# Performance work log

Hardware: AMD Instinct MI355X
Metric: run time of the kernel (lower is better)

The kernel has to match this reference:

```python
import jax, jax.numpy as jnp
import numpy as np

C = 1280  # layers_dim[1]


def setup_inputs() -> dict:
    key = jax.random.key(0)
    ks = jax.random.split(key, 8)
    E, N, H, W = 8192, 1024, 4, 4
    pose = jax.random.normal(ks[0], (E, 9), dtype=jnp.float32)
    image = jax.random.normal(ks[1], (N, C, H, W), dtype=jnp.float32)
    # edge_encoder params: Linear(9,1280) -> ReLU -> Linear(1280,2560) -> Sigmoid
    W1 = jax.random.normal(ks[2], (9, C), dtype=jnp.float32) * (1.0 / np.sqrt(9))
    b1 = jnp.zeros((C,), dtype=jnp.float32)
    W2 = jax.random.normal(ks[3], (C, 2 * C), dtype=jnp.float32) * (1.0 / np.sqrt(C))
    b2 = jnp.zeros((2 * C,), dtype=jnp.float32)
    src = jax.random.randint(ks[4], (E,), 0, N)
    dst = jax.random.randint(ks[5], (E,), 0, N)
    return {"pose": pose, "image": image, "W1": W1, "b1": b1,
            "W2": W2, "b2": b2, "src": src, "dst": dst}


def reference(pose, image, W1, b1, W2, b2, src, dst):
    # edge encoder: MLP -> sigmoid -> interleaved (gamma, beta) per channel
    h = jax.nn.relu(pose @ W1 + b1)                        # [E, C]
    e = jax.nn.sigmoid(h @ W2 + b2).reshape(-1, C, 2)      # [E, C, 2]
    gamma = e[:, :, 0][:, :, None, None]                   # [E, C, 1, 1]
    beta = e[:, :, 1][:, :, None, None]                    # [E, C, 1, 1]
    # per-edge message: affine transform of source node feature map
    m = gamma * image[src] + beta                          # [E, C, H, W]
    N = image.shape[0]
    s = jax.ops.segment_sum(m, dst, num_segments=N)        # [N, C, H, W]
    cnt = jax.ops.segment_sum(jnp.ones((m.shape[0],), m.dtype), dst,
                              num_segments=N)              # [N]
    cnt4 = cnt[:, None, None, None]
    # mean over mailbox; nodes with no incoming edges stay zero (DGL default)
    return jnp.where(cnt4 > 0, s / jnp.maximum(cnt4, 1.0), 0.0)
```

## Files before the change

kernel.cpp:

```cpp
#include <hip/hip_runtime.h>

#define C_DIM 1280
#define K_DIM 1280
#define N_DIM 2560
#define HWSZ 16
#define CHW (C_DIM*HWSZ)

#define BM 128
#define BN 128
#define BK 64
#define NT (K_DIM / BK)

#define EPB 32
#define NBC 2048

typedef __bf16 bf16;
typedef __attribute__((ext_vector_type(8))) __bf16 bf16x8;
typedef __attribute__((ext_vector_type(4))) __bf16 bf16x4;
typedef __attribute__((ext_vector_type(8))) unsigned short u16x8;
typedef __attribute__((ext_vector_type(4))) float f32x4;

__device__ __forceinline__ void gload_lds16(const void* g, void* l) {
  __builtin_amdgcn_global_load_lds(
      (const __attribute__((address_space(1))) void*)g,
      (__attribute__((address_space(3))) void*)l, 16, 0, 0);
}

__global__ __launch_bounds__(256) void prep(
    const float* __restrict__ pose, const float* __restrict__ W1,
    const float* __restrict__ b1, bf16* __restrict__ h,
    const float* __restrict__ W2, bf16* __restrict__ W2t,
    const float* __restrict__ img32, bf16* __restrict__ imgb,
    const int* __restrict__ dst, const int* __restrict__ src,
    int* __restrict__ offsets, int2* __restrict__ pairs, int E, int N)
{
  const int b = blockIdx.x;
  const int t = threadIdx.x;
  const int NBP = (E / EPB) * 5;
  const int NBT = (N_DIM / 32) * (K_DIM / 32);

  if (b == 0) {
    __shared__ int cnt[1024];
    __shared__ int cur[1024];
    __shared__ int wsum[4];
    #pragma unroll
    for (int i = 0; i < 4; ++i) cnt[t + 256 * i] = 0;
    __syncthreads();
    const int4* dst4 = (const int4*)dst;
    const int4* src4 = (const int4*)src;
    const int E4 = E >> 2;
    for (int e4 = t; e4 < E4; e4 += 256) {
      const int4 d = dst4[e4];
      atomicAdd(&cnt[d.x], 1); atomicAdd(&cnt[d.y], 1);
      atomicAdd(&cnt[d.z], 1); atomicAdd(&cnt[d.w], 1);
    }
    __syncthreads();
    const int s0 = cnt[4*t], s1 = cnt[4*t+1], s2 = cnt[4*t+2], s3 = cnt[4*t+3];
    const int tot = s0 + s1 + s2 + s3;
    const int lane = t & 63, w = t >> 6;
    int x = tot;
    #pragma unroll
    for (int off = 1; off < 64; off <<= 1) {
      int y = __shfl_up(x, off);
      if (lane >= off) x += y;
    }
    if (lane == 63) wsum[w] = x;
    __syncthreads();
    int woff = 0;
    for (int i = 0; i < w; ++i) woff += wsum[i];
    const int excl = x + woff - tot;
    const int o0 = excl, o1 = o0 + s0, o2 = o1 + s1, o3 = o2 + s2;
    offsets[4*t] = o0; offsets[4*t+1] = o1; offsets[4*t+2] = o2; offsets[4*t+3] = o3;
    cur[4*t] = o0; cur[4*t+1] = o1; cur[4*t+2] = o2; cur[4*t+3] = o3;
    if (t == 0) offsets[N] = E;
    __syncthreads();
    for (int e4 = t; e4 < E4; e4 += 256) {
      const int4 d = dst4[e4];
      const int4 s = src4[e4];
      const int e = e4 * 4;
      int p;
      p = atomicAdd(&cur[d.x], 1); pairs[p] = make_int2(e,     s.x);
      p = atomicAdd(&cur[d.y], 1); pairs[p] = make_int2(e + 1, s.y);
      p = atomicAdd(&cur[d.z], 1); pairs[p] = make_int2(e + 2, s.z);
      p = atomicAdd(&cur[d.w], 1); pairs[p] = make_int2(e + 3, s.w);
    }
    return;
  }

  const int pb = b - 1;
  if (pb < NBP) {
    const int eg = pb / 5;
    const int cc = pb % 5;
    const int c  = cc * 256 + t;
    const int e0 = eg * EPB;
    float w[9];
    #pragma unroll
    for (int k = 0; k < 9; ++k) w[k] = W1[k * C_DIM + c];
    const float bias = b1[c];
    #pragma unroll 4
    for (int i = 0; i < EPB; ++i) {
      const float* p = pose + (size_t)(e0 + i) * 9;
      float s = bias;
      #pragma unroll
      for (int k = 0; k < 9; ++k) s += p[k] * w[k];
      s = s > 0.f ? s : 0.f;
      h[(size_t)(e0 + i) * C_DIM + c] = (bf16)s;
    }
    return;
  }

  if (pb < NBP + NBT) {
    const int tb = pb - NBP;
    __shared__ float tile[32][33];
    const int n0 = (tb % (N_DIM / 32)) * 32;
    const int k0 = (tb / (N_DIM / 32)) * 32;
    const int r  = t >> 3;
    const int c4 = (t & 7) * 4;
    const f32x4 v = *(const f32x4*)(W2 + (size_t)(k0 + r) * N_DIM + n0 + c4);
    tile[r][c4] = v[0]; tile[r][c4+1] = v[1]; tile[r][c4+2] = v[2]; tile[r][c4+3] = v[3];
    __syncthreads();
    bf16x4 o;
    o[0] = (bf16)tile[c4+0][r];
    o[1] = (bf16)tile[c4+1][r];
    o[2] = (bf16)tile[c4+2][r];
    o[3] = (bf16)tile[c4+3][r];
    *(bf16x4*)(W2t + (size_t)(n0 + r) * K_DIM + k0 + c4) = o;
    return;
  }

  const int cb = pb - NBP - NBT;
  const int NCHUNK = (N * CHW) / 2048;
  for (int ch = cb; ch < NCHUNK; ch += NBC) {
    const size_t i = ((size_t)ch * 256 + t) * 8;
    const f32x4 a = *(const f32x4*)(img32 + i);
    const f32x4 bb = *(const f32x4*)(img32 + i + 4);
    bf16x8 o;
    o[0]=(bf16)a[0]; o[1]=(bf16)a[1]; o[2]=(bf16)a[2]; o[3]=(bf16)a[3];
    o[4]=(bf16)bb[0]; o[5]=(bf16)bb[1]; o[6]=(bf16)bb[2]; o[7]=(bf16)bb[3];
    *(bf16x8*)(imgb + i) = o;
  }
}

__global__ __launch_bounds__(256) void gemm_sigmoid(
    const bf16* __restrict__ A, const bf16* __restrict__ Bt,
    const float* __restrict__ b2, bf16* __restrict__ Eo)
{
  __shared__ __align__(16) char As[BM * BK * 2];
  __shared__ __align__(16) char Bs[BN * BK * 2];

  const int tid  = threadIdx.x;
  const int lane = tid & 63;
  const int wave = tid >> 6;
  const int wm   = wave >> 1;
  const int wn   = wave & 1;
  const int fr   = lane & 15;
  const int q    = lane >> 4;
  const int sw   = fr & 7;
  const int g0   = ((q ^ sw) << 4);
  const int g1   = (((4 + q) ^ sw) << 4);

  const int swzb = (blockIdx.x & 7) * 160 + (blockIdx.x >> 3);
  const int mb   = swzb / (N_DIM / BN);
  const int nb   = swzb % (N_DIM / BN);
  const long bm  = (long)mb * BM;
  const long bn  = (long)nb * BN;

  const bf16* Agl = A  + bm * K_DIM;
  const bf16* Bgl = Bt + bn * K_DIM;

  f32x4 acc[4][4];
  #pragma unroll
  for (int m = 0; m < 4; m++)
    #pragma unroll
    for (int n = 0; n < 4; n++) acc[m][n] = f32x4{0.f, 0.f, 0.f, 0.f};

  for (int t = 0; t < NT; ++t) {
    const int k0 = t * BK;
    #pragma unroll
    for (int i = 0; i < 4; ++i) {
      const int G   = i * 256 + tid;
      const int row = G >> 3, g = G & 7;
      const int kg  = (g ^ (row & 7)) << 3;
      gload_lds16(Agl + (size_t)row * K_DIM + k0 + kg, As + (size_t)G * 16);
      gload_lds16(Bgl + (size_t)row * K_DIM + k0 + kg, Bs + (size_t)G * 16);
    }
    asm volatile("s_waitcnt vmcnt(0)" ::: "memory");
    __syncthreads();

    bf16x8 a[4][2], b[4][2];
    #pragma unroll
    for (int m = 0; m < 4; ++m) {
      const int ra = (wm * 64 + m * 16 + fr) << 7;
      a[m][0] = *(const bf16x8*)(As + ra + g0);
      a[m][1] = *(const bf16x8*)(As + ra + g1);
    }
    #pragma unroll
    for (int n = 0; n < 4; ++n) {
      const int rb = (wn * 64 + n * 16 + fr) << 7;
      b[n][0] = *(const bf16x8*)(Bs + rb + g0);
      b[n][1] = *(const bf16x8*)(Bs + rb + g1);
    }
    __builtin_amdgcn_s_setprio(1);
    #pragma unroll
    for (int m = 0; m < 4; ++m)
      #pragma unroll
      for (int n = 0; n < 4; ++n) {
        acc[m][n] = __builtin_amdgcn_mfma_f32_16x16x32_bf16(a[m][0], b[n][0], acc[m][n], 0, 0, 0);
        acc[m][n] = __builtin_amdgcn_mfma_f32_16x16x32_bf16(a[m][1], b[n][1], acc[m][n], 0, 0, 0);
      }
    __builtin_amdgcn_s_setprio(0);
    __syncthreads();
  }

  #pragma unroll
  for (int m = 0; m < 4; ++m) {
    const long rowb = bm + wm * 64 + m * 16 + q * 4;
    #pragma unroll
    for (int n = 0; n < 4; ++n) {
      const long col = bn + wn * 64 + n * 16 + fr;
      const float bias = b2[col];
      #pragma unroll
      for (int r = 0; r < 4; ++r) {
        float v = acc[m][n][r] + bias;
        Eo[(rowb + r) * N_DIM + col] = (bf16)(1.f / (1.f + __expf(-v)));
      }
    }
  }
}

__global__ __launch_bounds__(256) void scatter_mean(
    const ushort* __restrict__ Eo,
    const ushort* __restrict__ imgb16,
    const int2* __restrict__ pairs,
    const int* __restrict__ offsets,
    float* __restrict__ out)
{
  const int n = blockIdx.x;
  const int c0 = blockIdx.y * 128;
  const int t = threadIdx.x;
  const int q = t & 1;
  const int cl = t >> 1;
  const int ca = c0 + cl;
  const int ioff = ca * HWSZ + q * 8;

  const int beg = offsets[n], end = offsets[n + 1];
  f32x4 aA0{0.f,0.f,0.f,0.f}, aA1{0.f,0.f,0.f,0.f};
  f32x4 aB0{0.f,0.f,0.f,0.f}, aB1{0.f,0.f,0.f,0.f};

  int2 p0{0,0}, p1{0,0};
  if (beg < end) p0 = pairs[beg];
  if (beg + 1 < end) p1 = pairs[beg + 1];

  auto edge = [&](int2 cp, f32x4& x0, f32x4& x1) {
    const u16x8 iv = *(const u16x8*)(imgb16 + (size_t)cp.y * CHW + ioff);
    const uint u = *(const uint*)(Eo + (size_t)cp.x * N_DIM + 2 * ca);
    const float g  = __uint_as_float(u << 16);
    const float be = __uint_as_float(u & 0xffff0000u);
    f32x4 i0, i1;
    i0[0] = __uint_as_float((uint)iv[0] << 16);
    i0[1] = __uint_as_float((uint)iv[1] << 16);
    i0[2] = __uint_as_float((uint)iv[2] << 16);
    i0[3] = __uint_as_float((uint)iv[3] << 16);
    i1[0] = __uint_as_float((uint)iv[4] << 16);
    i1[1] = __uint_as_float((uint)iv[5] << 16);
    i1[2] = __uint_as_float((uint)iv[6] << 16);
    i1[3] = __uint_as_float((uint)iv[7] << 16);
    x0 += g * i0 + be;
    x1 += g * i1 + be;
  };

  int ei = beg;
  for (; ei + 1 < end; ei += 2) {
    const int2 c0p = p0, c1p = p1;
    if (ei + 2 < end) p0 = pairs[ei + 2];
    if (ei + 3 < end) p1 = pairs[ei + 3];
    edge(c0p, aA0, aA1);
    edge(c1p, aB0, aB1);
  }
  if (ei < end) edge(p0, aA0, aA1);

  const int cnt = end - beg;
  const float inv = cnt > 0 ? 1.f / (float)cnt : 0.f;
  const f32x4 r0 = (aA0 + aB0) * inv;
  const f32x4 r1 = (aA1 + aB1) * inv;
  float* ob = out + (size_t)n * CHW + ioff;
  __builtin_nontemporal_store(r0, (f32x4*)ob);
  __builtin_nontemporal_store(r1, (f32x4*)(ob + 4));
}

extern "C" void kernel_launch(void* const* d_in, const int* in_sizes, int n_in,
                              void* d_out, int out_size, void* d_ws, size_t ws_size,
                              hipStream_t stream) {
  const float* pose  = (const float*)d_in[0];
  const float* image = (const float*)d_in[1];
  const float* W1    = (const float*)d_in[2];
  const float* b1    = (const float*)d_in[3];
  const float* W2    = (const float*)d_in[4];
  const float* b2    = (const float*)d_in[5];
  const int*   src   = (const int*)d_in[6];
  const int*   dst   = (const int*)d_in[7];
  const int E = in_sizes[6];
  const int N = in_sizes[1] / CHW;
  float* out = (float*)d_out;

  char* ws = (char*)d_ws;
  size_t off = 0;
  auto alloc = [&](size_t bytes) {
    void* p = ws + off;
    off = (off + bytes + 255) & ~(size_t)255;
    return p;
  };
  bf16* h     = (bf16*)alloc((size_t)E * C_DIM * sizeof(bf16));
  bf16* W2t   = (bf16*)alloc((size_t)N_DIM * K_DIM * sizeof(bf16));
  bf16* Eout  = (bf16*)alloc((size_t)E * N_DIM * sizeof(bf16));
  bf16* imgb  = (bf16*)alloc((size_t)N * CHW * sizeof(bf16));
  int* offs   = (int*)alloc((size_t)(N + 1) * sizeof(int));
  int2* pairs = (int2*)alloc((size_t)E * sizeof(int2));

  const int nb_prep = 1 + (E / EPB) * 5 + (N_DIM / 32) * (K_DIM / 32) + NBC;
  prep<<<nb_prep, 256, 0, stream>>>(pose, W1, b1, h, W2, W2t, image, imgb,
                                    dst, src, offs, pairs, E, N);

  gemm_sigmoid<<<(E / BM) * (N_DIM / BN), 256, 0, stream>>>(h, W2t, b2, Eout);

  scatter_mean<<<dim3(N, 10), 256, 0, stream>>>(
      (const ushort*)Eout, (const ushort*)imgb, pairs, offs, out);
}
```

Baseline: 154.7 us.

## Double-buffer GEMM with 256x320 tiles, 8 waves, and phased prefetch

The GEMM now uses 256x320 block tiles with 512 threads, double-buffered LDS, and loads for the next K-tile issued across four compute phases with explicit waitcnt and sched barriers. The goal is to hide global-to-LDS latency behind MFMA work and raise arithmetic intensity per block. The image conversion loop in prep is also unrolled to issue five loads before converting. The risks are higher register and LDS pressure (about 147KB of LDS per block), and a grid of only 256 blocks, which may leave CUs underused.

```diff
diff --git a/kernel.cpp b/kernel.cpp
--- a/kernel.cpp
+++ b/kernel.cpp
@@ -6,10 +6,10 @@
 #define HWSZ 16
 #define CHW (C_DIM*HWSZ)
 
-#define BM 128
-#define BN 128
-#define BK 64
-#define NT (K_DIM / BK)
+#define GBM 256
+#define GBN 320
+#define GBK 64
+#define GNT (K_DIM / GBK)
 
 #define EPB 32
 #define NBC 2048
@@ -20,11 +20,15 @@
 typedef __attribute__((ext_vector_type(8))) unsigned short u16x8;
 typedef __attribute__((ext_vector_type(4))) float f32x4;
 
+template<int V> struct IC { static constexpr int v = V; };
+
 __device__ __forceinline__ void gload_lds16(const void* g, void* l) {
   __builtin_amdgcn_global_load_lds(
       (const __attribute__((address_space(1))) void*)g,
       (__attribute__((address_space(3))) void*)l, 16, 0, 0);
 }
+
+#define SB __builtin_amdgcn_sched_barrier(0)
 
 __global__ __launch_bounds__(256) void prep(
     const float* __restrict__ pose, const float* __restrict__ W1,
@@ -129,95 +133,152 @@
   }
 
   const int cb = pb - NBP - NBT;
-  const int NCHUNK = (N * CHW) / 2048;
-  for (int ch = cb; ch < NCHUNK; ch += NBC) {
-    const size_t i = ((size_t)ch * 256 + t) * 8;
-    const f32x4 a = *(const f32x4*)(img32 + i);
-    const f32x4 bb = *(const f32x4*)(img32 + i + 4);
+  f32x4 va[5], vb[5];
+  #pragma unroll
+  for (int j = 0; j < 5; ++j) {
+    const size_t i = ((size_t)(cb + j * NBC) * 256 + t) * 8;
+    va[j] = *(const f32x4*)(img32 + i);
+    vb[j] = *(const f32x4*)(img32 + i + 4);
+  }
+  #pragma unroll
+  for (int j = 0; j < 5; ++j) {
+    const size_t i = ((size_t)(cb + j * NBC) * 256 + t) * 8;
     bf16x8 o;
-    o[0]=(bf16)a[0]; o[1]=(bf16)a[1]; o[2]=(bf16)a[2]; o[3]=(bf16)a[3];
-    o[4]=(bf16)bb[0]; o[5]=(bf16)bb[1]; o[6]=(bf16)bb[2]; o[7]=(bf16)bb[3];
+    o[0]=(bf16)va[j][0]; o[1]=(bf16)va[j][1]; o[2]=(bf16)va[j][2]; o[3]=(bf16)va[j][3];
+    o[4]=(bf16)vb[j][0]; o[5]=(bf16)vb[j][1]; o[6]=(bf16)vb[j][2]; o[7]=(bf16)vb[j][3];
     *(bf16x8*)(imgb + i) = o;
   }
 }
 
-__global__ __launch_bounds__(256) void gemm_sigmoid(
+__global__ __launch_bounds__(512, 2) void gemm_sigmoid(
     const bf16* __restrict__ A, const bf16* __restrict__ Bt,
     const float* __restrict__ b2, bf16* __restrict__ Eo)
 {
-  __shared__ __align__(16) char As[BM * BK * 2];
-  __shared__ __align__(16) char Bs[BN * BK * 2];
+  __shared__ __align__(16) char Asm[2][GBM * GBK * 2];
+  __shared__ __align__(16) char Bsm[2][GBN * GBK * 2];
 
   const int tid  = threadIdx.x;
   const int lane = tid & 63;
-  const int wave = tid >> 6;
-  const int wm   = wave >> 1;
-  const int wn   = wave & 1;
+  const int wid  = tid >> 6;
+  const int wr   = wid >> 2;
+  const int wc   = wid & 3;
   const int fr   = lane & 15;
   const int q    = lane >> 4;
   const int sw   = fr & 7;
   const int g0   = ((q ^ sw) << 4);
   const int g1   = (((4 + q) ^ sw) << 4);
 
-  const int swzb = (blockIdx.x & 7) * 160 + (blockIdx.x >> 3);
-  const int mb   = swzb / (N_DIM / BN);
-  const int nb   = swzb % (N_DIM / BN);
-  const long bm  = (long)mb * BM;
-  const long bn  = (long)nb * BN;
+  const int swzb = (blockIdx.x & 7) * 32 + (blockIdx.x >> 3);
+  const int mb   = swzb >> 3;
+  const int nb   = swzb & 7;
+  const long bm  = (long)mb * GBM;
+  const long bn  = (long)nb * GBN;
 
   const bf16* Agl = A  + bm * K_DIM;
   const bf16* Bgl = Bt + bn * K_DIM;
 
-  f32x4 acc[4][4];
+  f32x4 acc[8][5];
   #pragma unroll
-  for (int m = 0; m < 4; m++)
-    #pragma unroll
-    for (int n = 0; n < 4; n++) acc[m][n] = f32x4{0.f, 0.f, 0.f, 0.f};
-
-  for (int t = 0; t < NT; ++t) {
-    const int k0 = t * BK;
-    #pragma unroll
-    for (int i = 0; i < 4; ++i) {
-      const int G   = i * 256 + tid;
-      const int row = G >> 3, g = G & 7;
-      const int kg  = (g ^ (row & 7)) << 3;
-      gload_lds16(Agl + (size_t)row * K_DIM + k0 + kg, As + (size_t)G * 16);
-      gload_lds16(Bgl + (size_t)row * K_DIM + k0 + kg, Bs + (size_t)G * 16);
-    }
-    asm volatile("s_waitcnt vmcnt(0)" ::: "memory");
-    __syncthreads();
-
-    bf16x8 a[4][2], b[4][2];
-    #pragma unroll
-    for (int m = 0; m < 4; ++m) {
-      const int ra = (wm * 64 + m * 16 + fr) << 7;
-      a[m][0] = *(const bf16x8*)(As + ra + g0);
-      a[m][1] = *(const bf16x8*)(As + ra + g1);
-    }
-    #pragma unroll
-    for (int n = 0; n < 4; ++n) {
-      const int rb = (wn * 64 + n * 16 + fr) << 7;
-      b[n][0] = *(const bf16x8*)(Bs + rb + g0);
-      b[n][1] = *(const bf16x8*)(Bs + rb + g1);
-    }
-    __builtin_amdgcn_s_setprio(1);
-    #pragma unroll
-    for (int m = 0; m < 4; ++m)
+  for (int m = 0; m < 8; m++)
+    #pragma unroll
+    for (int n = 0; n < 5; n++) acc[m][n] = f32x4{0.f, 0.f, 0.f, 0.f};
+
+  auto STAGE_A = [&](int tt, int buf, int u) {
+    const int G = u * 512 + tid;
+    const int row = G >> 3, g = G & 7;
+    const int kg = (g ^ (row & 7)) << 3;
+    gload_lds16(Agl + (size_t)row * K_DIM + tt * GBK + kg, Asm[buf] + (size_t)G * 16);
+  };
+  auto STAGE_B = [&](int tt, int buf, int u) {
+    const int G = u * 512 + tid;
+    const int row = G >> 3, g = G & 7;
+    const int kg = (g ^ (row & 7)) << 3;
+    gload_lds16(Bgl + (size_t)row * K_DIM + tt * GBK + kg, Bsm[buf] + (size_t)G * 16);
+  };
+
+  STAGE_B(0,0,0); STAGE_B(0,0,1); STAGE_A(0,0,0);
+  STAGE_B(0,0,2); STAGE_B(0,0,3); STAGE_A(0,0,2); STAGE_B(0,0,4);
+  STAGE_A(0,0,1); STAGE_A(0,0,3);
+  asm volatile("s_waitcnt vmcnt(2)" ::: "memory");
+  SB;
+  __builtin_amdgcn_s_barrier();
+  SB;
+
+  auto tile_body = [&](auto PFc, int t) {
+    constexpr bool PF = (bool)decltype(PFc)::v;
+    const int cur = t & 1;
+    const int nxt = cur ^ 1;
+    const int tn  = t + 1;
+    const char* Ab = Asm[cur];
+    const char* Bb = Bsm[cur];
+
+    bf16x8 bfr[5][2];
+
+    auto do_phase = [&](auto Pc) {
+      constexpr int p = decltype(Pc)::v;
+      if constexpr (p == 0) {
+        #pragma unroll
+        for (int n = 0; n < 5; ++n) {
+          const int rb = (wc * 80 + n * 16 + fr) << 7;
+          bfr[n][0] = *(const bf16x8*)(Bb + rb + g0);
+          bfr[n][1] = *(const bf16x8*)(Bb + rb + g1);
+        }
+      }
+      bf16x8 a[2][2];
       #pragma unroll
-      for (int n = 0; n < 4; ++n) {
-        acc[m][n] = __builtin_amdgcn_mfma_f32_16x16x32_bf16(a[m][0], b[n][0], acc[m][n], 0, 0, 0);
-        acc[m][n] = __builtin_amdgcn_mfma_f32_16x16x32_bf16(a[m][1], b[n][1], acc[m][n], 0, 0, 0);
-      }
-    __builtin_amdgcn_s_setprio(0);
-    __syncthreads();
-  }
+      for (int mm = 0; mm < 2; ++mm) {
+        const int ra = (wr * 128 + (2 * p + mm) * 16 + fr) << 7;
+        a[mm][0] = *(const bf16x8*)(Ab + ra + g0);
+        a[mm][1] = *(const bf16x8*)(Ab + ra + g1);
+      }
+      if constexpr (PF) {
+        if constexpr (p == 0) { STAGE_B(tn,nxt,0); STAGE_B(tn,nxt,1); STAGE_A(tn,nxt,0); }
+        if constexpr (p == 1) { STAGE_B(tn,nxt,2); STAGE_B(tn,nxt,3); STAGE_A(tn,nxt,2); STAGE_B(tn,nxt,4); }
+        if constexpr (p == 2) { STAGE_A(tn,nxt,1); }
+        if constexpr (p == 3) { STAGE_A(tn,nxt,3); }
+      }
+      SB;
+      __builtin_amdgcn_s_barrier();
+      asm volatile("s_waitcnt lgkmcnt(0)" ::: "memory");
+      SB;
+      __builtin_amdgcn_s_setprio(1);
+      #pragma unroll
+      for (int mm = 0; mm < 2; ++mm)
+        #pragma unroll
+        for (int n = 0; n < 5; ++n) {
+          acc[2*p+mm][n] = __builtin_amdgcn_mfma_f32_16x16x32_bf16(a[mm][0], bfr[n][0], acc[2*p+mm][n], 0, 0, 0);
+          acc[2*p+mm][n] = __builtin_amdgcn_mfma_f32_16x16x32_bf16(a[mm][1], bfr[n][1], acc[2*p+mm][n], 0, 0, 0);
+        }
+      __builtin_amdgcn_s_setprio(0);
+      SB;
+      if constexpr (p == 1) {
+        if constexpr (PF) asm volatile("s_waitcnt vmcnt(7)" ::: "memory");
+        else              asm volatile("s_waitcnt vmcnt(0)" ::: "memory");
+        SB;
+      }
+      if constexpr (p == 3 && PF) {
+        asm volatile("s_waitcnt vmcnt(2)" ::: "memory");
+        SB;
+      }
+      __builtin_amdgcn_s_barrier();
+      SB;
+    };
+
+    do_phase(IC<0>{});
+    do_phase(IC<1>{});
+    do_phase(IC<2>{});
+    do_phase(IC<3>{});
+  };
+
+  for (int t = 0; t < GNT - 1; ++t) tile_body(IC<1>{}, t);
+  tile_body(IC<0>{}, GNT - 1);
 
   #pragma unroll
-  for (int m = 0; m < 4; ++m) {
-    const long rowb = bm + wm * 64 + m * 16 + q * 4;
-    #pragma unroll
-    for (int n = 0; n < 4; ++n) {
-      const long col = bn + wn * 64 + n * 16 + fr;
+  for (int m = 0; m < 8; ++m) {
+    const long rowb = bm + wr * 128 + m * 16 + q * 4;
+    #pragma unroll
+    for (int n = 0; n < 5; ++n) {
+      const long col = bn + wc * 80 + n * 16 + fr;
       const float bias = b2[col];
       #pragma unroll
       for (int r = 0; r < 4; ++r) {
@@ -321,7 +382,7 @@
   prep<<<nb_prep, 256, 0, stream>>>(pose, W1, b1, h, W2, W2t, image, imgb,
                                     dst, src, offs, pairs, E, N);
 
-  gemm_sigmoid<<<(E / BM) * (N_DIM / BN), 256, 0, stream>>>(h, W2t, b2, Eout);
+  gemm_sigmoid<<<(E / GBM) * (N_DIM / GBN), 512, 0, stream>>>(h, W2t, b2, Eout);
 
   scatter_mean<<<dim3(N, 10), 256, 0, stream>>>(
       (const ushort*)Eout, (const ushort*)imgb, pairs, offs, out);
```

Result: faster. 142.8 us (-7.7%).
